# Performance work log

Hardware: AMD Instinct MI355X
Metric: run time of the kernel (lower is better)

Reference implementation:

```python
import jax, jax.numpy as jnp
import numpy as np

B, S, D, H, E, K = 2, 1024, 1024, 2048, 8, 2


def setup_inputs() -> dict:
    key = jax.random.key(0)
    k1, k2, k3, k4 = jax.random.split(key, 4)
    x = jax.random.normal(k1, (B, S, D), dtype=jnp.float32)
    # router initialized to zeros in the module; use small random weights so
    # top-k routing is non-degenerate for a correctness baseline
    router_w = 0.02 * jax.random.normal(k2, (E, D), dtype=jnp.float32)
    router_b = jnp.zeros((E,), dtype=jnp.float32)
    w12 = 0.02 * jax.random.normal(k3, (E, D, 2 * H), dtype=jnp.float32)
    w3 = 0.02 * jax.random.normal(k4, (E, H, D), dtype=jnp.float32)
    return {"x": x, "router_w": router_w, "router_b": router_b, "w12": w12, "w3": w3}


def reference(x, router_w, router_b, w12, w3):
    # Router (eval mode: no jitter noise)
    logits = jnp.einsum("bsd,ed->bse", x, router_w) + router_b      # [B,S,E]
    scores = jax.nn.sigmoid(logits)
    top_vals, top_idx = jax.lax.top_k(scores, K)                     # [B,S,K]
    rweights = top_vals / (jnp.sum(top_vals, axis=-1, keepdims=True) + 1e-6)
    # per-expert combine weight: sum over top-k slots where idx == e
    onehot = jax.nn.one_hot(top_idx, E, dtype=x.dtype)               # [B,S,K,E]
    combine = jnp.einsum("bsk,bske->bse", rweights, onehot)          # [B,S,E]
    # Dense per-expert SwiGLU over all tokens (matches naive module math)
    h12 = jnp.einsum("bsd,edh->ebsh", x, w12)                        # [E,B,S,2H]
    h1, h2 = jnp.split(h12, 2, axis=-1)
    hidden = jax.nn.silu(h1) * h2                                    # [E,B,S,H]
    expert_out = jnp.einsum("ebsh,ehd->ebsd", hidden, w3)            # [E,B,S,D]
    out = jnp.einsum("ebsd,bse->bsd", expert_out, combine)           # [B,S,D]
    aux_loss = 0.01 * jnp.mean(logits ** 2)
    return out, aux_loss
```

## Files before the change

### kernel.cpp

```cpp
#include <hip/hip_runtime.h>
#include <math.h>
#include <stdint.h>

#define B_ 2
#define S_ 1024
#define D_ 1024
#define H_ 2048
#define E_ 8
#define TOK_ (B_*S_)
#define N1_ (2*H_)
#define PAIRS_ (TOK_*2)
#define MAXTILES_ 40

typedef float f32x4 __attribute__((ext_vector_type(4)));
typedef short short8 __attribute__((ext_vector_type(8)));

__device__ __forceinline__ unsigned short f2bf(float f) {
  unsigned int u = __float_as_uint(f);
  u += 0x7fffu + ((u >> 16) & 1u);
  return (unsigned short)(u >> 16);
}
__device__ __forceinline__ float bf2f(unsigned short u) {
  return __uint_as_float(((unsigned int)u) << 16);
}

__global__ __launch_bounds__(256) void transpose_f32_to_bf16(
    const float* __restrict__ src, unsigned short* __restrict__ dst, int R, int C)
{
  __shared__ float tile[64][65];
  const int e = blockIdx.z;
  const float* s = src + (size_t)e * R * C;
  unsigned short* d = dst + (size_t)e * R * C;
  const int c0 = blockIdx.x * 64, r0 = blockIdx.y * 64;
  const int lrow = threadIdx.x >> 4;
  const int lc4  = threadIdx.x & 15;
#pragma unroll
  for (int i = 0; i < 4; ++i) {
    int r = lrow + i * 16;
    float4 v = *(const float4*)&s[(size_t)(r0 + r) * C + c0 + lc4 * 4];
    tile[r][lc4 * 4 + 0] = v.x;
    tile[r][lc4 * 4 + 1] = v.y;
    tile[r][lc4 * 4 + 2] = v.z;
    tile[r][lc4 * 4 + 3] = v.w;
  }
  __syncthreads();
  const int rx = (threadIdx.x & 15) * 4;
  const int cy = threadIdx.x >> 4;
#pragma unroll
  for (int i = 0; i < 4; ++i) {
    int c = cy + i * 16;
    ushort4 o;
    o.x = f2bf(tile[rx + 0][c]);
    o.y = f2bf(tile[rx + 1][c]);
    o.z = f2bf(tile[rx + 2][c]);
    o.w = f2bf(tile[rx + 3][c]);
    *(ushort4*)&d[(size_t)(c0 + c) * R + r0 + rx] = o;
  }
}

__global__ __launch_bounds__(256) void router_kernel(
    const float* __restrict__ x, const float* __restrict__ rw,
    const float* __restrict__ rb, int* __restrict__ counts,
    int* __restrict__ expert_of, int* __restrict__ slot_of,
    float* __restrict__ w_of, float* __restrict__ tok_ssq)
{
  const int wave = threadIdx.x >> 6, lane = threadIdx.x & 63;
  const int t = blockIdx.x * 4 + wave;
  const float4* x4 = (const float4*)(x + (size_t)t * D_);
  const float4* rw4 = (const float4*)rw;
  float acc[E_];
#pragma unroll
  for (int e = 0; e < E_; ++e) acc[e] = 0.f;
#pragma unroll
  for (int d4 = 0; d4 < D_ / 4 / 64; ++d4) {
    int idx = d4 * 64 + lane;
    float4 xv = x4[idx];
#pragma unroll
    for (int e = 0; e < E_; ++e) {
      float4 wv = rw4[e * (D_ / 4) + idx];
      acc[e] += xv.x * wv.x + xv.y * wv.y + xv.z * wv.z + xv.w * wv.w;
    }
  }
#pragma unroll
  for (int e = 0; e < E_; ++e) {
    float v = acc[e];
#pragma unroll
    for (int sh = 32; sh > 0; sh >>= 1) v += __shfl_xor(v, sh, 64);
    acc[e] = v;
  }
  if (lane == 0) {
    float logits[E_], sc[E_], ssq = 0.f;
#pragma unroll
    for (int e = 0; e < E_; ++e) {
      logits[e] = acc[e] + rb[e];
      ssq += logits[e] * logits[e];
      sc[e] = 1.f / (1.f + __expf(-logits[e]));
    }
    tok_ssq[t] = ssq;
    int i1 = 0;
#pragma unroll
    for (int e = 1; e < E_; ++e) if (sc[e] > sc[i1]) i1 = e;
    int i2 = (i1 == 0) ? 1 : 0;
#pragma unroll
    for (int e = 0; e < E_; ++e)
      if (e != i1 && e != i2 && sc[e] > sc[i2]) i2 = e;
    float v1 = sc[i1], v2 = sc[i2];
    float inv = 1.f / (v1 + v2 + 1e-6f);
    int s1 = atomicAdd(&counts[i1], 1);
    int s2 = atomicAdd(&counts[i2], 1);
    expert_of[t * 2]     = i1; slot_of[t * 2]     = s1; w_of[t * 2]     = v1 * inv;
    expert_of[t * 2 + 1] = i2; slot_of[t * 2 + 1] = s2; w_of[t * 2 + 1] = v2 * inv;
  }
}

__global__ __launch_bounds__(256) void meta_kernel(
    const int* __restrict__ counts, const float* __restrict__ tok_ssq,
    int* __restrict__ offsets, int* __restrict__ tile_e, int* __restrict__ tile_m0,
    float* __restrict__ out_aux)
{
  if (threadIdx.x == 0) {
    int o = 0, nt = 0;
    for (int e = 0; e < E_; ++e) {
      offsets[e] = o;
      for (int m0 = 0; m0 < counts[e]; m0 += 128) {
        tile_e[nt] = e; tile_m0[nt] = m0; ++nt;
      }
      o += counts[e];
    }
    for (; nt < MAXTILES_; ++nt) tile_e[nt] = -1;
  }
  __shared__ float sm[256];
  float s = 0.f;
  for (int i = threadIdx.x; i < TOK_; i += 256) s += tok_ssq[i];
  sm[threadIdx.x] = s;
  __syncthreads();
  for (int h = 128; h > 0; h >>= 1) {
    if (threadIdx.x < h) sm[threadIdx.x] += sm[threadIdx.x + h];
    __syncthreads();
  }
  if (threadIdx.x == 0) *out_aux = 0.01f * sm[0] / (float)(TOK_ * E_);
}

__global__ __launch_bounds__(256) void pack_kernel(
    const float* __restrict__ x, const int* __restrict__ expert_of,
    const int* __restrict__ slot_of, const int* __restrict__ offsets,
    unsigned short* __restrict__ px, int* __restrict__ pair_row)
{
  const int pair = blockIdx.x;
  const int t = pair >> 1;
  const int e = expert_of[pair];
  const int row = offsets[e] + slot_of[pair];
  if (threadIdx.x == 0) pair_row[pair] = row;
  const float4* xr = (const float4*)(x + (size_t)t * D_);
  ushort4* pr = (ushort4*)(px + (size_t)row * D_);
  float4 v = xr[threadIdx.x];
  ushort4 o;
  o.x = f2bf(v.x); o.y = f2bf(v.y); o.z = f2bf(v.z); o.w = f2bf(v.w);
  pr[threadIdx.x] = o;
}

__device__ __forceinline__ void stage64(const unsigned short* gbase, int gstride,
                                        unsigned short* sbase, int kk,
                                        int wave, int lane)
{
  const int rw = lane >> 3;
  const int seg = (lane & 7) ^ rw;
#pragma unroll
  for (int c = 0; c < 4; ++c) {
    int row = wave * 8 + c * 32 + rw;
    const unsigned short* g = gbase + (size_t)row * gstride + kk + seg * 8;
    unsigned short* s = sbase + (size_t)(wave * 8 + c * 32) * 64;
    __builtin_amdgcn_global_load_lds(
        (const __attribute__((address_space(1))) void*)g,
        (__attribute__((address_space(3))) void*)s, 16, 0, 0);
  }
}

__device__ __forceinline__ void stage64_clamped(const unsigned short* gbase, int gstride,
                                                int row0, int rowmax,
                                                unsigned short* sbase, int kk,
                                                int wave, int lane)
{
  const int rw = lane >> 3;
  const int seg = (lane & 7) ^ rw;
#pragma unroll
  for (int c = 0; c < 4; ++c) {
    int row = row0 + wave * 8 + c * 32 + rw;
    row = (row < rowmax) ? row : rowmax - 1;
    const unsigned short* g = gbase + (size_t)row * gstride + kk + seg * 8;
    unsigned short* s = sbase + (size_t)(wave * 8 + c * 32) * 64;
    __builtin_amdgcn_global_load_lds(
        (const __attribute__((address_space(1))) void*)g,
        (__attribute__((address_space(3))) void*)s, 16, 0, 0);
  }
}

__device__ __forceinline__ short8 read_frag64(const unsigned short* smem, int row,
                                              int j, int lk) {
  const int s = (j * 4 + lk) ^ (row & 7);
  return *(const short8*)&smem[row * 64 + s * 8];
}

__global__ __launch_bounds__(256, 2) void gemm1_kernel(
    const unsigned short* __restrict__ px, const unsigned short* __restrict__ w12t,
    unsigned short* __restrict__ hid, const int* __restrict__ counts,
    const int* __restrict__ offsets, const int* __restrict__ tile_e,
    const int* __restrict__ tile_m0)
{
  const int ti = blockIdx.y, nt = blockIdx.x;
  const int e = tile_e[ti];
  if (e < 0) return;
  const int m0 = tile_m0[ti];
  const int cnt = counts[e];
  const int off = offsets[e];
  const int tid = threadIdx.x;
  const int wave = tid >> 6, lane = tid & 63;
  const int wm = wave >> 1, wn = wave & 1;
  const int lr = lane & 15, lk = lane >> 4;

  __shared__ __align__(16) unsigned short As[128 * 64];
  __shared__ __align__(16) unsigned short B1s[128 * 64];
  __shared__ __align__(16) unsigned short B2s[128 * 64];

  f32x4 zero = {0.f, 0.f, 0.f, 0.f};
  f32x4 acc1[4][4], acc2[4][4];
#pragma unroll
  for (int mi = 0; mi < 4; ++mi)
#pragma unroll
    for (int ni = 0; ni < 4; ++ni) { acc1[mi][ni] = zero; acc2[mi][ni] = zero; }

  const unsigned short* B1base = w12t + ((size_t)e * N1_ + nt * 128) * D_;
  const unsigned short* B2base = w12t + ((size_t)e * N1_ + H_ + nt * 128) * D_;

  for (int kk = 0; kk < D_; kk += 64) {
    stage64_clamped(px, D_, off + m0, PAIRS_, As, kk, wave, lane);
    stage64(B1base, D_, B1s, kk, wave, lane);
    stage64(B2base, D_, B2s, kk, wave, lane);
    __syncthreads();
#pragma unroll
    for (int j = 0; j < 2; ++j) {
      short8 a[4], b1[4], b2[4];
#pragma unroll
      for (int i = 0; i < 4; ++i) {
        a[i]  = read_frag64(As,  wm * 64 + i * 16 + lr, j, lk);
        b1[i] = read_frag64(B1s, wn * 64 + i * 16 + lr, j, lk);
        b2[i] = read_frag64(B2s, wn * 64 + i * 16 + lr, j, lk);
      }
#pragma unroll
      for (int mi = 0; mi < 4; ++mi)
#pragma unroll
        for (int ni = 0; ni < 4; ++ni) {
          acc1[mi][ni] = __builtin_amdgcn_mfma_f32_16x16x32_bf16(a[mi], b1[ni], acc1[mi][ni], 0, 0, 0);
          acc2[mi][ni] = __builtin_amdgcn_mfma_f32_16x16x32_bf16(a[mi], b2[ni], acc2[mi][ni], 0, 0, 0);
        }
    }
    __syncthreads();
  }

#pragma unroll
  for (int mi = 0; mi < 4; ++mi)
#pragma unroll
    for (int r = 0; r < 4; ++r) {
      int row_local = m0 + wm * 64 + mi * 16 + lk * 4 + r;
      if (row_local < cnt) {
#pragma unroll
        for (int ni = 0; ni < 4; ++ni) {
          int col = nt * 128 + wn * 64 + ni * 16 + lr;
          float v1 = acc1[mi][ni][r];
          float v2 = acc2[mi][ni][r];
          float hval = (v1 / (1.f + __expf(-v1))) * v2;
          hid[(size_t)(off + row_local) * H_ + col] = f2bf(hval);
        }
      }
    }
}

__global__ __launch_bounds__(256, 4) void gemm2_kernel(
    const unsigned short* __restrict__ hid, const unsigned short* __restrict__ w3t,
    const int* __restrict__ counts, const int* __restrict__ offsets,
    const int* __restrict__ tile_e, const int* __restrict__ tile_m0,
    unsigned short* __restrict__ ybuf)
{
  const int ti = blockIdx.y, nt = blockIdx.x, ks = blockIdx.z;
  const int e = tile_e[ti];
  if (e < 0) return;
  const int m0 = tile_m0[ti];
  const int cnt = counts[e];
  const int off = offsets[e];
  const int tid = threadIdx.x;
  const int wave = tid >> 6, lane = tid & 63;
  const int wm = wave >> 1, wn = wave & 1;
  const int lr = lane & 15, lk = lane >> 4;

  __shared__ __align__(16) unsigned short As[128 * 64];
  __shared__ __align__(16) unsigned short Bs[128 * 64];

  f32x4 zero = {0.f, 0.f, 0.f, 0.f};
  f32x4 acc[4][4];
#pragma unroll
  for (int mi = 0; mi < 4; ++mi)
#pragma unroll
    for (int ni = 0; ni < 4; ++ni) acc[mi][ni] = zero;

  const unsigned short* Bbase = w3t + ((size_t)e * D_ + nt * 128) * H_;
  unsigned short* yb = ybuf + (size_t)ks * PAIRS_ * D_;

  const int k0 = ks * (H_ / 2), k1 = k0 + (H_ / 2);
  for (int kk = k0; kk < k1; kk += 64) {
    stage64_clamped(hid, H_, off + m0, PAIRS_, As, kk, wave, lane);
    stage64(Bbase, H_, Bs, kk, wave, lane);
    __syncthreads();
#pragma unroll
    for (int j = 0; j < 2; ++j) {
      short8 a[4], b[4];
#pragma unroll
      for (int i = 0; i < 4; ++i) {
        a[i] = read_frag64(As, wm * 64 + i * 16 + lr, j, lk);
        b[i] = read_frag64(Bs, wn * 64 + i * 16 + lr, j, lk);
      }
#pragma unroll
      for (int mi = 0; mi < 4; ++mi)
#pragma unroll
        for (int ni = 0; ni < 4; ++ni)
          acc[mi][ni] = __builtin_amdgcn_mfma_f32_16x16x32_bf16(a[mi], b[ni], acc[mi][ni], 0, 0, 0);
    }
    __syncthreads();
  }

#pragma unroll
  for (int mi = 0; mi < 4; ++mi)
#pragma unroll
    for (int r = 0; r < 4; ++r) {
      int row_local = m0 + wm * 64 + mi * 16 + lk * 4 + r;
      if (row_local < cnt) {
        int g = off + row_local;
#pragma unroll
        for (int ni = 0; ni < 4; ++ni) {
          int col = nt * 128 + wn * 64 + ni * 16 + lr;
          yb[(size_t)g * D_ + col] = f2bf(acc[mi][ni][r]);
        }
      }
    }
}

__global__ __launch_bounds__(256) void combine_kernel(
    const unsigned short* __restrict__ ybuf, const int* __restrict__ pair_row,
    const float* __restrict__ w_of, float* __restrict__ out)
{
  const int t = blockIdx.x;
  const int r0 = pair_row[t * 2], r1 = pair_row[t * 2 + 1];
  const float w0 = w_of[t * 2], w1 = w_of[t * 2 + 1];
  const unsigned short* y1p = ybuf + (size_t)PAIRS_ * D_;
  const int i = threadIdx.x;
  ushort4 a0 = *(const ushort4*)&ybuf[(size_t)r0 * D_ + i * 4];
  ushort4 b0 = *(const ushort4*)&y1p [(size_t)r0 * D_ + i * 4];
  ushort4 a1 = *(const ushort4*)&ybuf[(size_t)r1 * D_ + i * 4];
  ushort4 b1 = *(const ushort4*)&y1p [(size_t)r1 * D_ + i * 4];
  float4 o;
  o.x = w0 * (bf2f(a0.x) + bf2f(b0.x)) + w1 * (bf2f(a1.x) + bf2f(b1.x));
  o.y = w0 * (bf2f(a0.y) + bf2f(b0.y)) + w1 * (bf2f(a1.y) + bf2f(b1.y));
  o.z = w0 * (bf2f(a0.z) + bf2f(b0.z)) + w1 * (bf2f(a1.z) + bf2f(b1.z));
  o.w = w0 * (bf2f(a0.w) + bf2f(b0.w)) + w1 * (bf2f(a1.w) + bf2f(b1.w));
  ((float4*)out)[(size_t)t * (D_ / 4) + i] = o;
}

extern "C" void kernel_launch(void* const* d_in, const int* in_sizes, int n_in,
                              void* d_out, int out_size, void* d_ws, size_t ws_size,
                              hipStream_t stream)
{
  const float* x   = (const float*)d_in[0];
  const float* rw  = (const float*)d_in[1];
  const float* rb  = (const float*)d_in[2];
  const float* w12 = (const float*)d_in[3];
  const float* w3  = (const float*)d_in[4];
  float* out = (float*)d_out;

  char* wsb = (char*)d_ws;
  int*   counts    = (int*)(wsb + 0);
  int*   offsets   = (int*)(wsb + 64);
  int*   tile_e    = (int*)(wsb + 128);
  int*   tile_m0   = (int*)(wsb + 384);
  int*   expert_of = (int*)(wsb + 1024);
  int*   slot_of   = (int*)(wsb + 1024 + 16384);
  float* w_of      = (float*)(wsb + 1024 + 2 * 16384);
  int*   pair_row  = (int*)(wsb + 1024 + 3 * 16384);
  float* tok_ssq   = (float*)(wsb + 1024 + 4 * 16384);
  unsigned short* px   = (unsigned short*)(wsb + (128 << 10));
  unsigned short* hid  = (unsigned short*)(wsb + (128 << 10) + ((size_t)8  << 20));
  unsigned short* w12t = (unsigned short*)(wsb + (128 << 10) + ((size_t)24 << 20));
  unsigned short* w3t  = (unsigned short*)(wsb + (128 << 10) + ((size_t)88 << 20));
  unsigned short* ybuf = (unsigned short*)(wsb + (128 << 10) + ((size_t)120 << 20));

  hipMemsetAsync(counts, 0, E_ * sizeof(int), stream);

  transpose_f32_to_bf16<<<dim3(N1_ / 64, D_ / 64, E_), 256, 0, stream>>>(w12, w12t, D_, N1_);
  transpose_f32_to_bf16<<<dim3(D_ / 64, H_ / 64, E_), 256, 0, stream>>>(w3, w3t, H_, D_);
  router_kernel<<<TOK_ / 4, 256, 0, stream>>>(x, rw, rb, counts, expert_of, slot_of, w_of, tok_ssq);
  meta_kernel<<<1, 256, 0, stream>>>(counts, tok_ssq, offsets, tile_e, tile_m0, out + (size_t)TOK_ * D_);
  pack_kernel<<<PAIRS_, 256, 0, stream>>>(x, expert_of, slot_of, offsets, px, pair_row);
  gemm1_kernel<<<dim3(16, MAXTILES_), 256, 0, stream>>>(px, w12t, hid, counts, offsets, tile_e, tile_m0);
  gemm2_kernel<<<dim3(8, MAXTILES_, 2), 256, 0, stream>>>(hid, w3t, counts, offsets, tile_e, tile_m0, ybuf);
  combine_kernel<<<TOK_, 256, 0, stream>>>(ybuf, pair_row, w_of, out);
}
```

Measured before the change: 417.7 us.

## Fuse combine into gemm2 epilogue via weighted atomic adds to output

Removes the separate combine kernel and the bf16 ybuf intermediate. gemm2 now scales each result by its routing weight and atomically adds it into the zeroed fp32 output, using a new row-to-pair map written by the pack kernel. This removes an intermediate write and read round-trip and one launch. In exchange it adds an output memset and many global float atomics with contention from the two K-splits and two experts. The occupancy hint for gemm2 is also lowered.

Result: slower. 434.7 us (+4.1%).

```diff
diff --git a/kernel.cpp b/kernel.cpp
--- a/kernel.cpp
+++ b/kernel.cpp
@@ -20,9 +20,6 @@
   u += 0x7fffu + ((u >> 16) & 1u);
   return (unsigned short)(u >> 16);
 }
-__device__ __forceinline__ float bf2f(unsigned short u) {
-  return __uint_as_float(((unsigned int)u) << 16);
-}
 
 __global__ __launch_bounds__(256) void transpose_f32_to_bf16(
     const float* __restrict__ src, unsigned short* __restrict__ dst, int R, int C)
@@ -144,13 +141,13 @@
 __global__ __launch_bounds__(256) void pack_kernel(
     const float* __restrict__ x, const int* __restrict__ expert_of,
     const int* __restrict__ slot_of, const int* __restrict__ offsets,
-    unsigned short* __restrict__ px, int* __restrict__ pair_row)
+    unsigned short* __restrict__ px, int* __restrict__ row_pair)
 {
   const int pair = blockIdx.x;
   const int t = pair >> 1;
   const int e = expert_of[pair];
   const int row = offsets[e] + slot_of[pair];
-  if (threadIdx.x == 0) pair_row[pair] = row;
+  if (threadIdx.x == 0) row_pair[row] = pair;
   const float4* xr = (const float4*)(x + (size_t)t * D_);
   ushort4* pr = (ushort4*)(px + (size_t)row * D_);
   float4 v = xr[threadIdx.x];
@@ -275,11 +272,12 @@
     }
 }
 
-__global__ __launch_bounds__(256, 4) void gemm2_kernel(
+__global__ __launch_bounds__(256, 3) void gemm2_kernel(
     const unsigned short* __restrict__ hid, const unsigned short* __restrict__ w3t,
     const int* __restrict__ counts, const int* __restrict__ offsets,
     const int* __restrict__ tile_e, const int* __restrict__ tile_m0,
-    unsigned short* __restrict__ ybuf)
+    const int* __restrict__ row_pair, const float* __restrict__ w_of,
+    float* __restrict__ out)
 {
   const int ti = blockIdx.y, nt = blockIdx.x, ks = blockIdx.z;
   const int e = tile_e[ti];
@@ -303,7 +301,6 @@
     for (int ni = 0; ni < 4; ++ni) acc[mi][ni] = zero;
 
   const unsigned short* Bbase = w3t + ((size_t)e * D_ + nt * 128) * H_;
-  unsigned short* yb = ybuf + (size_t)ks * PAIRS_ * D_;
 
   const int k0 = ks * (H_ / 2), k1 = k0 + (H_ / 2);
   for (int kk = k0; kk < k1; kk += 64) {
@@ -334,34 +331,16 @@
       int row_local = m0 + wm * 64 + mi * 16 + lk * 4 + r;
       if (row_local < cnt) {
         int g = off + row_local;
+        int pr = row_pair[g];
+        float wgt = w_of[pr];
+        float* op = out + (size_t)(pr >> 1) * D_;
 #pragma unroll
         for (int ni = 0; ni < 4; ++ni) {
           int col = nt * 128 + wn * 64 + ni * 16 + lr;
-          yb[(size_t)g * D_ + col] = f2bf(acc[mi][ni][r]);
+          atomicAdd(&op[col], wgt * acc[mi][ni][r]);
         }
       }
     }
-}
-
-__global__ __launch_bounds__(256) void combine_kernel(
-    const unsigned short* __restrict__ ybuf, const int* __restrict__ pair_row,
-    const float* __restrict__ w_of, float* __restrict__ out)
-{
-  const int t = blockIdx.x;
-  const int r0 = pair_row[t * 2], r1 = pair_row[t * 2 + 1];
-  const float w0 = w_of[t * 2], w1 = w_of[t * 2 + 1];
-  const unsigned short* y1p = ybuf + (size_t)PAIRS_ * D_;
-  const int i = threadIdx.x;
-  ushort4 a0 = *(const ushort4*)&ybuf[(size_t)r0 * D_ + i * 4];
-  ushort4 b0 = *(const ushort4*)&y1p [(size_t)r0 * D_ + i * 4];
-  ushort4 a1 = *(const ushort4*)&ybuf[(size_t)r1 * D_ + i * 4];
-  ushort4 b1 = *(const ushort4*)&y1p [(size_t)r1 * D_ + i * 4];
-  float4 o;
-  o.x = w0 * (bf2f(a0.x) + bf2f(b0.x)) + w1 * (bf2f(a1.x) + bf2f(b1.x));
-  o.y = w0 * (bf2f(a0.y) + bf2f(b0.y)) + w1 * (bf2f(a1.y) + bf2f(b1.y));
-  o.z = w0 * (bf2f(a0.z) + bf2f(b0.z)) + w1 * (bf2f(a1.z) + bf2f(b1.z));
-  o.w = w0 * (bf2f(a0.w) + bf2f(b0.w)) + w1 * (bf2f(a1.w) + bf2f(b1.w));
-  ((float4*)out)[(size_t)t * (D_ / 4) + i] = o;
 }
 
 extern "C" void kernel_launch(void* const* d_in, const int* in_sizes, int n_in,
@@ -383,22 +362,21 @@
   int*   expert_of = (int*)(wsb + 1024);
   int*   slot_of   = (int*)(wsb + 1024 + 16384);
   float* w_of      = (float*)(wsb + 1024 + 2 * 16384);
-  int*   pair_row  = (int*)(wsb + 1024 + 3 * 16384);
+  int*   row_pair  = (int*)(wsb + 1024 + 3 * 16384);
   float* tok_ssq   = (float*)(wsb + 1024 + 4 * 16384);
   unsigned short* px   = (unsigned short*)(wsb + (128 << 10));
   unsigned short* hid  = (unsigned short*)(wsb + (128 << 10) + ((size_t)8  << 20));
   unsigned short* w12t = (unsigned short*)(wsb + (128 << 10) + ((size_t)24 << 20));
   unsigned short* w3t  = (unsigned short*)(wsb + (128 << 10) + ((size_t)88 << 20));
-  unsigned short* ybuf = (unsigned short*)(wsb + (128 << 10) + ((size_t)120 << 20));
 
   hipMemsetAsync(counts, 0, E_ * sizeof(int), stream);
+  hipMemsetAsync(out, 0, (size_t)TOK_ * D_ * sizeof(float), stream);
 
   transpose_f32_to_bf16<<<dim3(N1_ / 64, D_ / 64, E_), 256, 0, stream>>>(w12, w12t, D_, N1_);
   transpose_f32_to_bf16<<<dim3(D_ / 64, H_ / 64, E_), 256, 0, stream>>>(w3, w3t, H_, D_);
   router_kernel<<<TOK_ / 4, 256, 0, stream>>>(x, rw, rb, counts, expert_of, slot_of, w_of, tok_ssq);
   meta_kernel<<<1, 256, 0, stream>>>(counts, tok_ssq, offsets, tile_e, tile_m0, out + (size_t)TOK_ * D_);
-  pack_kernel<<<PAIRS_, 256, 0, stream>>>(x, expert_of, slot_of, offsets, px, pair_row);
+  pack_kernel<<<PAIRS_, 256, 0, stream>>>(x, expert_of, slot_of, offsets, px, row_pair);
   gemm1_kernel<<<dim3(16, MAXTILES_), 256, 0, stream>>>(px, w12t, hid, counts, offsets, tile_e, tile_m0);
-  gemm2_kernel<<<dim3(8, MAXTILES_, 2), 256, 0, stream>>>(hid, w3t, counts, offsets, tile_e, tile_m0, ybuf);
-  combine_kernel<<<TOK_, 256, 0, stream>>>(ybuf, pair_row, w_of, out);
-}
+  gemm2_kernel<<<dim3(8, MAXTILES_, 2), 256, 0, stream>>>(hid, w3t, counts, offsets, tile_e, tile_m0, row_pair, w_of, out);
+}
```

## Double-buffer gemm1 LDS and widen its M tile to 256 rows

Applied to the files above, without the earlier changes.

Gemm1 now uses 512-thread blocks covering 256 routed rows per tile, with its own tile list built at 256-row granularity in meta_kernel. Each staged expert-weight tile is therefore reused across twice as many rows, reducing global traffic for the weight operands. Its LDS is double-buffered so the next K-slice is staged while MFMAs run on the current one. The cost is about 128KB of LDS per block, which likely limits each CU to one block, plus more padded rows for experts with small counts.

Result: slower. 441.1 us (+5.6%).

```diff
diff --git a/kernel.cpp b/kernel.cpp
--- a/kernel.cpp
+++ b/kernel.cpp
@@ -10,7 +10,8 @@
 #define TOK_ (B_*S_)
 #define N1_ (2*H_)
 #define PAIRS_ (TOK_*2)
-#define MAXTILES_ 40
+#define MAXT1_ 24
+#define MAXT2_ 40
 
 typedef float f32x4 __attribute__((ext_vector_type(4)));
 typedef short short8 __attribute__((ext_vector_type(8)));
@@ -115,19 +116,25 @@
 
 __global__ __launch_bounds__(256) void meta_kernel(
     const int* __restrict__ counts, const float* __restrict__ tok_ssq,
-    int* __restrict__ offsets, int* __restrict__ tile_e, int* __restrict__ tile_m0,
+    int* __restrict__ offsets,
+    int* __restrict__ tile1_e, int* __restrict__ tile1_m0,
+    int* __restrict__ tile2_e, int* __restrict__ tile2_m0,
     float* __restrict__ out_aux)
 {
   if (threadIdx.x == 0) {
-    int o = 0, nt = 0;
+    int o = 0, n1 = 0, n2 = 0;
     for (int e = 0; e < E_; ++e) {
       offsets[e] = o;
+      for (int m0 = 0; m0 < counts[e]; m0 += 256) {
+        tile1_e[n1] = e; tile1_m0[n1] = m0; ++n1;
+      }
       for (int m0 = 0; m0 < counts[e]; m0 += 128) {
-        tile_e[nt] = e; tile_m0[nt] = m0; ++nt;
+        tile2_e[n2] = e; tile2_m0[n2] = m0; ++n2;
       }
       o += counts[e];
     }
-    for (; nt < MAXTILES_; ++nt) tile_e[nt] = -1;
+    for (; n1 < MAXT1_; ++n1) tile1_e[n1] = -1;
+    for (; n2 < MAXT2_; ++n2) tile2_e[n2] = -1;
   }
   __shared__ float sm[256];
   float s = 0.f;
@@ -195,22 +202,58 @@
   }
 }
 
+__device__ __forceinline__ void stageA256(const unsigned short* gbase, int gstride,
+                                          int row0, int rowmax,
+                                          unsigned short* sbase, int kk,
+                                          int wave, int lane)
+{
+  const int rw = lane >> 3;
+  const int seg = (lane & 7) ^ rw;
+#pragma unroll
+  for (int c = 0; c < 4; ++c) {
+    int row = row0 + wave * 32 + c * 8 + rw;
+    row = (row < rowmax) ? row : rowmax - 1;
+    const unsigned short* g = gbase + (size_t)row * gstride + kk + seg * 8;
+    unsigned short* s = sbase + (size_t)(wave * 32 + c * 8) * 64;
+    __builtin_amdgcn_global_load_lds(
+        (const __attribute__((address_space(1))) void*)g,
+        (__attribute__((address_space(3))) void*)s, 16, 0, 0);
+  }
+}
+
+__device__ __forceinline__ void stageB128(const unsigned short* gbase, int gstride,
+                                          unsigned short* sbase, int kk,
+                                          int wave, int lane)
+{
+  const int rw = lane >> 3;
+  const int seg = (lane & 7) ^ rw;
+#pragma unroll
+  for (int c = 0; c < 2; ++c) {
+    int row = wave * 16 + c * 8 + rw;
+    const unsigned short* g = gbase + (size_t)row * gstride + kk + seg * 8;
+    unsigned short* s = sbase + (size_t)(wave * 16 + c * 8) * 64;
+    __builtin_amdgcn_global_load_lds(
+        (const __attribute__((address_space(1))) void*)g,
+        (__attribute__((address_space(3))) void*)s, 16, 0, 0);
+  }
+}
+
 __device__ __forceinline__ short8 read_frag64(const unsigned short* smem, int row,
                                               int j, int lk) {
   const int s = (j * 4 + lk) ^ (row & 7);
   return *(const short8*)&smem[row * 64 + s * 8];
 }
 
-__global__ __launch_bounds__(256, 2) void gemm1_kernel(
+__global__ __launch_bounds__(512, 2) void gemm1_kernel(
     const unsigned short* __restrict__ px, const unsigned short* __restrict__ w12t,
     unsigned short* __restrict__ hid, const int* __restrict__ counts,
-    const int* __restrict__ offsets, const int* __restrict__ tile_e,
-    const int* __restrict__ tile_m0)
+    const int* __restrict__ offsets, const int* __restrict__ tile1_e,
+    const int* __restrict__ tile1_m0)
 {
   const int ti = blockIdx.y, nt = blockIdx.x;
-  const int e = tile_e[ti];
+  const int e = tile1_e[ti];
   if (e < 0) return;
-  const int m0 = tile_m0[ti];
+  const int m0 = tile1_m0[ti];
   const int cnt = counts[e];
   const int off = offsets[e];
   const int tid = threadIdx.x;
@@ -218,9 +261,9 @@
   const int wm = wave >> 1, wn = wave & 1;
   const int lr = lane & 15, lk = lane >> 4;
 
-  __shared__ __align__(16) unsigned short As[128 * 64];
-  __shared__ __align__(16) unsigned short B1s[128 * 64];
-  __shared__ __align__(16) unsigned short B2s[128 * 64];
+  __shared__ __align__(16) unsigned short As[2][256 * 64];
+  __shared__ __align__(16) unsigned short B1s[2][128 * 64];
+  __shared__ __align__(16) unsigned short B2s[2][128 * 64];
 
   f32x4 zero = {0.f, 0.f, 0.f, 0.f};
   f32x4 acc1[4][4], acc2[4][4];
@@ -232,19 +275,27 @@
   const unsigned short* B1base = w12t + ((size_t)e * N1_ + nt * 128) * D_;
   const unsigned short* B2base = w12t + ((size_t)e * N1_ + H_ + nt * 128) * D_;
 
-  for (int kk = 0; kk < D_; kk += 64) {
-    stage64_clamped(px, D_, off + m0, PAIRS_, As, kk, wave, lane);
-    stage64(B1base, D_, B1s, kk, wave, lane);
-    stage64(B2base, D_, B2s, kk, wave, lane);
-    __syncthreads();
+  stageA256(px, D_, off + m0, PAIRS_, As[0], 0, wave, lane);
+  stageB128(B1base, D_, B1s[0], 0, wave, lane);
+  stageB128(B2base, D_, B2s[0], 0, wave, lane);
+  __syncthreads();
+
+  int cur = 0;
+  const int NSTEP = D_ / 64;
+  for (int t = 0; t < NSTEP; ++t) {
+    if (t + 1 < NSTEP) {
+      stageA256(px, D_, off + m0, PAIRS_, As[cur ^ 1], (t + 1) * 64, wave, lane);
+      stageB128(B1base, D_, B1s[cur ^ 1], (t + 1) * 64, wave, lane);
+      stageB128(B2base, D_, B2s[cur ^ 1], (t + 1) * 64, wave, lane);
+    }
 #pragma unroll
     for (int j = 0; j < 2; ++j) {
       short8 a[4], b1[4], b2[4];
 #pragma unroll
       for (int i = 0; i < 4; ++i) {
-        a[i]  = read_frag64(As,  wm * 64 + i * 16 + lr, j, lk);
-        b1[i] = read_frag64(B1s, wn * 64 + i * 16 + lr, j, lk);
-        b2[i] = read_frag64(B2s, wn * 64 + i * 16 + lr, j, lk);
+        a[i]  = read_frag64(As[cur],  wm * 64 + i * 16 + lr, j, lk);
+        b1[i] = read_frag64(B1s[cur], wn * 64 + i * 16 + lr, j, lk);
+        b2[i] = read_frag64(B2s[cur], wn * 64 + i * 16 + lr, j, lk);
       }
 #pragma unroll
       for (int mi = 0; mi < 4; ++mi)
@@ -255,6 +306,7 @@
         }
     }
     __syncthreads();
+    cur ^= 1;
   }
 
 #pragma unroll
@@ -278,13 +330,13 @@
 __global__ __launch_bounds__(256, 4) void gemm2_kernel(
     const unsigned short* __restrict__ hid, const unsigned short* __restrict__ w3t,
     const int* __restrict__ counts, const int* __restrict__ offsets,
-    const int* __restrict__ tile_e, const int* __restrict__ tile_m0,
+    const int* __restrict__ tile2_e, const int* __restrict__ tile2_m0,
     unsigned short* __restrict__ ybuf)
 {
   const int ti = blockIdx.y, nt = blockIdx.x, ks = blockIdx.z;
-  const int e = tile_e[ti];
+  const int e = tile2_e[ti];
   if (e < 0) return;
-  const int m0 = tile_m0[ti];
+  const int m0 = tile2_m0[ti];
   const int cnt = counts[e];
   const int off = offsets[e];
   const int tid = threadIdx.x;
@@ -378,8 +430,10 @@
   char* wsb = (char*)d_ws;
   int*   counts    = (int*)(wsb + 0);
   int*   offsets   = (int*)(wsb + 64);
-  int*   tile_e    = (int*)(wsb + 128);
-  int*   tile_m0   = (int*)(wsb + 384);
+  int*   tile2_e   = (int*)(wsb + 128);
+  int*   tile2_m0  = (int*)(wsb + 384);
+  int*   tile1_e   = (int*)(wsb + 640);
+  int*   tile1_m0  = (int*)(wsb + 768);
   int*   expert_of = (int*)(wsb + 1024);
   int*   slot_of   = (int*)(wsb + 1024 + 16384);
   float* w_of      = (float*)(wsb + 1024 + 2 * 16384);
@@ -396,9 +450,9 @@
   transpose_f32_to_bf16<<<dim3(N1_ / 64, D_ / 64, E_), 256, 0, stream>>>(w12, w12t, D_, N1_);
   transpose_f32_to_bf16<<<dim3(D_ / 64, H_ / 64, E_), 256, 0, stream>>>(w3, w3t, H_, D_);
   router_kernel<<<TOK_ / 4, 256, 0, stream>>>(x, rw, rb, counts, expert_of, slot_of, w_of, tok_ssq);
-  meta_kernel<<<1, 256, 0, stream>>>(counts, tok_ssq, offsets, tile_e, tile_m0, out + (size_t)TOK_ * D_);
+  meta_kernel<<<1, 256, 0, stream>>>(counts, tok_ssq, offsets, tile1_e, tile1_m0, tile2_e, tile2_m0, out + (size_t)TOK_ * D_);
   pack_kernel<<<PAIRS_, 256, 0, stream>>>(x, expert_of, slot_of, offsets, px, pair_row);
-  gemm1_kernel<<<dim3(16, MAXTILES_), 256, 0, stream>>>(px, w12t, hid, counts, offsets, tile_e, tile_m0);
-  gemm2_kernel<<<dim3(8, MAXTILES_, 2), 256, 0, stream>>>(hid, w3t, counts, offsets, tile_e, tile_m0, ybuf);
+  gemm1_kernel<<<dim3(16, MAXT1_), 512, 0, stream>>>(px, w12t, hid, counts, offsets, tile1_e, tile1_m0);
+  gemm2_kernel<<<dim3(8, MAXT2_, 2), 256, 0, stream>>>(hid, w3t, counts, offsets, tile2_e, tile2_m0, ybuf);
   combine_kernel<<<TOK_, 256, 0, stream>>>(ybuf, pair_row, w_of, out);
 }
```

## Fuse router with packing, merge transposes, use fixed per-expert capacity slots

Applied to the files above, without the earlier changes.

The two weight transposes are merged into one launch that also zeroes the expert counters, which replaces the memset. Token packing moves into the router kernel: the x row stays in registers and is written as bf16 to a slot at expert*TOK+slot, so the pack kernel and its second read of x go away. Giving each expert a fixed-capacity region removes the offsets prefix scan, but the px, hid and ybuf buffers grow to E*TOK rows and spread across much more workspace.

Result: no change. 420.1 us (+0.6%).

```diff
diff --git a/kernel.cpp b/kernel.cpp
--- a/kernel.cpp
+++ b/kernel.cpp
@@ -10,6 +10,7 @@
 #define TOK_ (B_*S_)
 #define N1_ (2*H_)
 #define PAIRS_ (TOK_*2)
+#define CAP_ (E_*TOK_)
 #define MAXTILES_ 40
 
 typedef float f32x4 __attribute__((ext_vector_type(4)));
@@ -24,16 +25,16 @@
   return __uint_as_float(((unsigned int)u) << 16);
 }
 
-__global__ __launch_bounds__(256) void transpose_f32_to_bf16(
-    const float* __restrict__ src, unsigned short* __restrict__ dst, int R, int C)
+__device__ __forceinline__ void transpose_tile(
+    const float* __restrict__ src, unsigned short* __restrict__ dst,
+    int R, int C, int e, int bx, int by, int tid)
 {
   __shared__ float tile[64][65];
-  const int e = blockIdx.z;
   const float* s = src + (size_t)e * R * C;
   unsigned short* d = dst + (size_t)e * R * C;
-  const int c0 = blockIdx.x * 64, r0 = blockIdx.y * 64;
-  const int lrow = threadIdx.x >> 4;
-  const int lc4  = threadIdx.x & 15;
+  const int c0 = bx * 64, r0 = by * 64;
+  const int lrow = tid >> 4;
+  const int lc4  = tid & 15;
 #pragma unroll
   for (int i = 0; i < 4; ++i) {
     int r = lrow + i * 16;
@@ -44,8 +45,8 @@
     tile[r][lc4 * 4 + 3] = v.w;
   }
   __syncthreads();
-  const int rx = (threadIdx.x & 15) * 4;
-  const int cy = threadIdx.x >> 4;
+  const int rx = (tid & 15) * 4;
+  const int cy = tid >> 4;
 #pragma unroll
   for (int i = 0; i < 4; ++i) {
     int c = cy + i * 16;
@@ -58,27 +59,46 @@
   }
 }
 
-__global__ __launch_bounds__(256) void router_kernel(
+__global__ __launch_bounds__(256) void transpose_all_kernel(
+    const float* __restrict__ w12, const float* __restrict__ w3,
+    unsigned short* __restrict__ w12t, unsigned short* __restrict__ w3t,
+    int* __restrict__ counts)
+{
+  const int bid = blockIdx.x, tid = threadIdx.x;
+  if (bid == 0 && tid < E_) counts[tid] = 0;
+  if (bid < 8192) {
+    int e = bid >> 10, rem = bid & 1023;
+    transpose_tile(w12, w12t, D_, N1_, e, rem & 63, rem >> 6, tid);
+  } else {
+    int b2 = bid - 8192;
+    int e = b2 >> 9, rem = b2 & 511;
+    transpose_tile(w3, w3t, H_, D_, e, rem & 15, rem >> 4, tid);
+  }
+}
+
+__global__ __launch_bounds__(256) void router_pack_kernel(
     const float* __restrict__ x, const float* __restrict__ rw,
     const float* __restrict__ rb, int* __restrict__ counts,
     int* __restrict__ expert_of, int* __restrict__ slot_of,
-    float* __restrict__ w_of, float* __restrict__ tok_ssq)
+    float* __restrict__ w_of, float* __restrict__ tok_ssq,
+    unsigned short* __restrict__ px)
 {
   const int wave = threadIdx.x >> 6, lane = threadIdx.x & 63;
   const int t = blockIdx.x * 4 + wave;
   const float4* x4 = (const float4*)(x + (size_t)t * D_);
   const float4* rw4 = (const float4*)rw;
+  float4 xv[4];
   float acc[E_];
 #pragma unroll
   for (int e = 0; e < E_; ++e) acc[e] = 0.f;
 #pragma unroll
-  for (int d4 = 0; d4 < D_ / 4 / 64; ++d4) {
+  for (int d4 = 0; d4 < 4; ++d4) {
     int idx = d4 * 64 + lane;
-    float4 xv = x4[idx];
+    xv[d4] = x4[idx];
 #pragma unroll
     for (int e = 0; e < E_; ++e) {
       float4 wv = rw4[e * (D_ / 4) + idx];
-      acc[e] += xv.x * wv.x + xv.y * wv.y + xv.z * wv.z + xv.w * wv.w;
+      acc[e] += xv[d4].x * wv.x + xv[d4].y * wv.y + xv[d4].z * wv.z + xv[d4].w * wv.w;
     }
   }
 #pragma unroll
@@ -88,6 +108,7 @@
     for (int sh = 32; sh > 0; sh >>= 1) v += __shfl_xor(v, sh, 64);
     acc[e] = v;
   }
+  int r1v = 0, r2v = 0;
   if (lane == 0) {
     float logits[E_], sc[E_], ssq = 0.f;
 #pragma unroll
@@ -110,25 +131,38 @@
     int s2 = atomicAdd(&counts[i2], 1);
     expert_of[t * 2]     = i1; slot_of[t * 2]     = s1; w_of[t * 2]     = v1 * inv;
     expert_of[t * 2 + 1] = i2; slot_of[t * 2 + 1] = s2; w_of[t * 2 + 1] = v2 * inv;
+    r1v = i1 * TOK_ + s1;
+    r2v = i2 * TOK_ + s2;
+  }
+  const int r1 = __shfl(r1v, 0), r2 = __shfl(r2v, 0);
+#pragma unroll
+  for (int d4 = 0; d4 < 4; ++d4) {
+    int idx = d4 * 64 + lane;
+    ushort4 o;
+    o.x = f2bf(xv[d4].x); o.y = f2bf(xv[d4].y);
+    o.z = f2bf(xv[d4].z); o.w = f2bf(xv[d4].w);
+    *(ushort4*)&px[(size_t)r1 * D_ + idx * 4] = o;
+    *(ushort4*)&px[(size_t)r2 * D_ + idx * 4] = o;
   }
 }
 
 __global__ __launch_bounds__(256) void meta_kernel(
     const int* __restrict__ counts, const float* __restrict__ tok_ssq,
-    int* __restrict__ offsets, int* __restrict__ tile_e, int* __restrict__ tile_m0,
-    float* __restrict__ out_aux)
+    const int* __restrict__ expert_of, const int* __restrict__ slot_of,
+    int* __restrict__ tile_e, int* __restrict__ tile_m0,
+    int* __restrict__ pair_row, float* __restrict__ out_aux)
 {
   if (threadIdx.x == 0) {
-    int o = 0, nt = 0;
+    int nt = 0;
     for (int e = 0; e < E_; ++e) {
-      offsets[e] = o;
       for (int m0 = 0; m0 < counts[e]; m0 += 128) {
         tile_e[nt] = e; tile_m0[nt] = m0; ++nt;
       }
-      o += counts[e];
     }
     for (; nt < MAXTILES_; ++nt) tile_e[nt] = -1;
   }
+  for (int p = threadIdx.x; p < PAIRS_; p += 256)
+    pair_row[p] = expert_of[p] * TOK_ + slot_of[p];
   __shared__ float sm[256];
   float s = 0.f;
   for (int i = threadIdx.x; i < TOK_; i += 256) s += tok_ssq[i];
@@ -141,24 +175,6 @@
   if (threadIdx.x == 0) *out_aux = 0.01f * sm[0] / (float)(TOK_ * E_);
 }
 
-__global__ __launch_bounds__(256) void pack_kernel(
-    const float* __restrict__ x, const int* __restrict__ expert_of,
-    const int* __restrict__ slot_of, const int* __restrict__ offsets,
-    unsigned short* __restrict__ px, int* __restrict__ pair_row)
-{
-  const int pair = blockIdx.x;
-  const int t = pair >> 1;
-  const int e = expert_of[pair];
-  const int row = offsets[e] + slot_of[pair];
-  if (threadIdx.x == 0) pair_row[pair] = row;
-  const float4* xr = (const float4*)(x + (size_t)t * D_);
-  ushort4* pr = (ushort4*)(px + (size_t)row * D_);
-  float4 v = xr[threadIdx.x];
-  ushort4 o;
-  o.x = f2bf(v.x); o.y = f2bf(v.y); o.z = f2bf(v.z); o.w = f2bf(v.w);
-  pr[threadIdx.x] = o;
-}
-
 __device__ __forceinline__ void stage64(const unsigned short* gbase, int gstride,
                                         unsigned short* sbase, int kk,
                                         int wave, int lane)
@@ -204,15 +220,14 @@
 __global__ __launch_bounds__(256, 2) void gemm1_kernel(
     const unsigned short* __restrict__ px, const unsigned short* __restrict__ w12t,
     unsigned short* __restrict__ hid, const int* __restrict__ counts,
-    const int* __restrict__ offsets, const int* __restrict__ tile_e,
-    const int* __restrict__ tile_m0)
+    const int* __restrict__ tile_e, const int* __restrict__ tile_m0)
 {
   const int ti = blockIdx.y, nt = blockIdx.x;
   const int e = tile_e[ti];
   if (e < 0) return;
   const int m0 = tile_m0[ti];
   const int cnt = counts[e];
-  const int off = offsets[e];
+  const int off = e * TOK_;
   const int tid = threadIdx.x;
   const int wave = tid >> 6, lane = tid & 63;
   const int wm = wave >> 1, wn = wave & 1;
@@ -233,7 +248,7 @@
   const unsigned short* B2base = w12t + ((size_t)e * N1_ + H_ + nt * 128) * D_;
 
   for (int kk = 0; kk < D_; kk += 64) {
-    stage64_clamped(px, D_, off + m0, PAIRS_, As, kk, wave, lane);
+    stage64_clamped(px, D_, off + m0, CAP_, As, kk, wave, lane);
     stage64(B1base, D_, B1s, kk, wave, lane);
     stage64(B2base, D_, B2s, kk, wave, lane);
     __syncthreads();
@@ -277,16 +292,15 @@
 
 __global__ __launch_bounds__(256, 4) void gemm2_kernel(
     const unsigned short* __restrict__ hid, const unsigned short* __restrict__ w3t,
-    const int* __restrict__ counts, const int* __restrict__ offsets,
-    const int* __restrict__ tile_e, const int* __restrict__ tile_m0,
-    unsigned short* __restrict__ ybuf)
+    const int* __restrict__ counts, const int* __restrict__ tile_e,
+    const int* __restrict__ tile_m0, unsigned short* __restrict__ ybuf)
 {
   const int ti = blockIdx.y, nt = blockIdx.x, ks = blockIdx.z;
   const int e = tile_e[ti];
   if (e < 0) return;
   const int m0 = tile_m0[ti];
   const int cnt = counts[e];
-  const int off = offsets[e];
+  const int off = e * TOK_;
   const int tid = threadIdx.x;
   const int wave = tid >> 6, lane = tid & 63;
   const int wm = wave >> 1, wn = wave & 1;
@@ -303,11 +317,11 @@
     for (int ni = 0; ni < 4; ++ni) acc[mi][ni] = zero;
 
   const unsigned short* Bbase = w3t + ((size_t)e * D_ + nt * 128) * H_;
-  unsigned short* yb = ybuf + (size_t)ks * PAIRS_ * D_;
+  unsigned short* yb = ybuf + (size_t)ks * CAP_ * D_;
 
   const int k0 = ks * (H_ / 2), k1 = k0 + (H_ / 2);
   for (int kk = k0; kk < k1; kk += 64) {
-    stage64_clamped(hid, H_, off + m0, PAIRS_, As, kk, wave, lane);
+    stage64_clamped(hid, H_, off + m0, CAP_, As, kk, wave, lane);
     stage64(Bbase, H_, Bs, kk, wave, lane);
     __syncthreads();
 #pragma unroll
@@ -350,7 +364,7 @@
   const int t = blockIdx.x;
   const int r0 = pair_row[t * 2], r1 = pair_row[t * 2 + 1];
   const float w0 = w_of[t * 2], w1 = w_of[t * 2 + 1];
-  const unsigned short* y1p = ybuf + (size_t)PAIRS_ * D_;
+  const unsigned short* y1p = ybuf + (size_t)CAP_ * D_;
   const int i = threadIdx.x;
   ushort4 a0 = *(const ushort4*)&ybuf[(size_t)r0 * D_ + i * 4];
   ushort4 b0 = *(const ushort4*)&y1p [(size_t)r0 * D_ + i * 4];
@@ -377,28 +391,23 @@
 
   char* wsb = (char*)d_ws;
   int*   counts    = (int*)(wsb + 0);
-  int*   offsets   = (int*)(wsb + 64);
-  int*   tile_e    = (int*)(wsb + 128);
-  int*   tile_m0   = (int*)(wsb + 384);
-  int*   expert_of = (int*)(wsb + 1024);
-  int*   slot_of   = (int*)(wsb + 1024 + 16384);
-  float* w_of      = (float*)(wsb + 1024 + 2 * 16384);
-  int*   pair_row  = (int*)(wsb + 1024 + 3 * 16384);
-  float* tok_ssq   = (float*)(wsb + 1024 + 4 * 16384);
-  unsigned short* px   = (unsigned short*)(wsb + (128 << 10));
-  unsigned short* hid  = (unsigned short*)(wsb + (128 << 10) + ((size_t)8  << 20));
-  unsigned short* w12t = (unsigned short*)(wsb + (128 << 10) + ((size_t)24 << 20));
-  unsigned short* w3t  = (unsigned short*)(wsb + (128 << 10) + ((size_t)88 << 20));
-  unsigned short* ybuf = (unsigned short*)(wsb + (128 << 10) + ((size_t)120 << 20));
-
-  hipMemsetAsync(counts, 0, E_ * sizeof(int), stream);
-
-  transpose_f32_to_bf16<<<dim3(N1_ / 64, D_ / 64, E_), 256, 0, stream>>>(w12, w12t, D_, N1_);
-  transpose_f32_to_bf16<<<dim3(D_ / 64, H_ / 64, E_), 256, 0, stream>>>(w3, w3t, H_, D_);
-  router_kernel<<<TOK_ / 4, 256, 0, stream>>>(x, rw, rb, counts, expert_of, slot_of, w_of, tok_ssq);
-  meta_kernel<<<1, 256, 0, stream>>>(counts, tok_ssq, offsets, tile_e, tile_m0, out + (size_t)TOK_ * D_);
-  pack_kernel<<<PAIRS_, 256, 0, stream>>>(x, expert_of, slot_of, offsets, px, pair_row);
-  gemm1_kernel<<<dim3(16, MAXTILES_), 256, 0, stream>>>(px, w12t, hid, counts, offsets, tile_e, tile_m0);
-  gemm2_kernel<<<dim3(8, MAXTILES_, 2), 256, 0, stream>>>(hid, w3t, counts, offsets, tile_e, tile_m0, ybuf);
+  int*   tile_e    = (int*)(wsb + 1024);
+  int*   tile_m0   = (int*)(wsb + 2048);
+  int*   expert_of = (int*)(wsb + 4096);
+  int*   slot_of   = (int*)(wsb + 4096 + 16384);
+  float* w_of      = (float*)(wsb + 4096 + 2 * 16384);
+  int*   pair_row  = (int*)(wsb + 4096 + 3 * 16384);
+  float* tok_ssq   = (float*)(wsb + 4096 + 4 * 16384);
+  unsigned short* px   = (unsigned short*)(wsb + ((size_t)1   << 20));
+  unsigned short* hid  = (unsigned short*)(wsb + ((size_t)34  << 20));
+  unsigned short* w12t = (unsigned short*)(wsb + ((size_t)98  << 20));
+  unsigned short* w3t  = (unsigned short*)(wsb + ((size_t)162 << 20));
+  unsigned short* ybuf = (unsigned short*)(wsb + ((size_t)194 << 20));
+
+  transpose_all_kernel<<<12288, 256, 0, stream>>>(w12, w3, w12t, w3t, counts);
+  router_pack_kernel<<<TOK_ / 4, 256, 0, stream>>>(x, rw, rb, counts, expert_of, slot_of, w_of, tok_ssq, px);
+  meta_kernel<<<1, 256, 0, stream>>>(counts, tok_ssq, expert_of, slot_of, tile_e, tile_m0, pair_row, out + (size_t)TOK_ * D_);
+  gemm1_kernel<<<dim3(16, MAXTILES_), 256, 0, stream>>>(px, w12t, hid, counts, tile_e, tile_m0);
+  gemm2_kernel<<<dim3(8, MAXTILES_, 2), 256, 0, stream>>>(hid, w3t, counts, tile_e, tile_m0, ybuf);
   combine_kernel<<<TOK_, 256, 0, stream>>>(ybuf, pair_row, w_of, out);
 }
```
